# Kernel tuning notes

Measured on AMD Instinct MI355X. Metric: run time of the kernel, lower is better.

Reference implementation:

```python
import jax, jax.numpy as jnp
import numpy as np

N, DEG, IN_DIM, HID, OUT = 50000, 32, 256, 256, 128

def setup_inputs() -> dict:
    key = jax.random.key(0)
    k1, k2, k3, k4, k5, k6 = jax.random.split(key, 6)
    node_features = jax.random.normal(k1, (N, IN_DIM), dtype=jnp.float32)
    neighbor_idx = jax.random.randint(k2, (N, DEG), 0, N)
    scale1 = 1.0 / np.sqrt(2 * IN_DIM)
    scale2 = 1.0 / np.sqrt(HID)
    W1 = jax.random.normal(k3, (HID, 2 * IN_DIM), dtype=jnp.float32) * scale1
    b1 = jax.random.normal(k4, (HID,), dtype=jnp.float32) * scale1
    W2 = jax.random.normal(k5, (OUT, HID), dtype=jnp.float32) * scale2
    b2 = jax.random.normal(k6, (OUT,), dtype=jnp.float32) * scale2
    return {"node_features": node_features, "neighbor_idx": neighbor_idx,
            "W1": W1, "b1": b1, "W2": W2, "b2": b2}

def reference(node_features, neighbor_idx, W1, b1, W2, b2):
    # Layer 0 (mean aggregator, with neighbors):
    # gather [N, DEG, IN_DIM] neighbor features, mean over DEG
    nbr_mean = jnp.mean(node_features[neighbor_idx], axis=1)  # [N, IN_DIM]
    combined = jnp.concatenate([node_features, nbr_mean], axis=-1)  # [N, 2*IN_DIM]
    h = jax.nn.relu(combined @ W1.T + b1)  # [N, HID]
    # Layer 1: empty neighbor list -> linear_without_neighbors + relu
    out = jax.nn.relu(h @ W2.T + b2)  # [N, OUT]
    return out
```

## Files before the change

### kernel.cpp

```cpp
#include <hip/hip_runtime.h>
#include <stdint.h>

#define N_NODES 50000
#define DEG     32
#define IN_DIM  256
#define K1      512
#define HID     256
#define OUT_DIM 128

#define NCHUNK  4
#define CDIM    64
#define SLICE8  ((size_t)N_NODES * CDIM)
#define GT      16

#define MT2    64
#define NT2B   ((N_NODES + MT2 - 1) / MT2)
#define KC     64
#define HSTR2  264

typedef __bf16 bf16x8 __attribute__((ext_vector_type(8)));
typedef float  f32x4  __attribute__((ext_vector_type(4)));
typedef float  f32x2  __attribute__((ext_vector_type(2)));

__device__ __forceinline__ unsigned short f2bf(float f) {
    union { float f; unsigned u; } v; v.f = f;
    unsigned r = v.u + 0x7fffu + ((v.u >> 16) & 1u);
    return (unsigned short)(r >> 16);
}
__device__ __forceinline__ int clampN(int v) {
    return v < 0 ? 0 : (v >= N_NODES ? N_NODES - 1 : v);
}
__device__ __forceinline__ void async_copy16(const void* g, void* l) {
    __builtin_amdgcn_global_load_lds(
        (const __attribute__((address_space(1))) void*)g,
        (__attribute__((address_space(3))) void*)l, 16, 0, 0);
}

#define FEAT_BLKS ((N_NODES + 7) / 8)
__global__ __launch_bounds__(256)
void prep_all(const float* __restrict__ feat,
              const float* __restrict__ W1, const float* __restrict__ W2,
              const int*   __restrict__ nbr,
              unsigned short* __restrict__ featb,
              unsigned char*  __restrict__ featF8,
              unsigned short* __restrict__ W1b, unsigned short* __restrict__ W2b,
              unsigned short* __restrict__ nbr16)
{
    const int t = threadIdx.x;
    if (blockIdx.x < FEAT_BLKS) {
        const int node = blockIdx.x * 8 + (t >> 5);
        const int seg  = t & 31;
        if (node < N_NODES) {
            const float4* src = (const float4*)(feat + (size_t)node * IN_DIM + seg * 8);
            float4 f0 = src[0], f1 = src[1];
            ushort4 o0, o1;
            o0.x = f2bf(f0.x); o0.y = f2bf(f0.y); o0.z = f2bf(f0.z); o0.w = f2bf(f0.w);
            o1.x = f2bf(f1.x); o1.y = f2bf(f1.y); o1.z = f2bf(f1.z); o1.w = f2bf(f1.w);
            unsigned short* db = featb + (size_t)node * IN_DIM + seg * 8;
            *(ushort4*)db       = o0;
            *(ushort4*)(db + 4) = o1;
            int u0 = 0, u1 = 0;
            u0 = __builtin_amdgcn_cvt_pk_fp8_f32(f0.x, f0.y, u0, false);
            u0 = __builtin_amdgcn_cvt_pk_fp8_f32(f0.z, f0.w, u0, true);
            u1 = __builtin_amdgcn_cvt_pk_fp8_f32(f1.x, f1.y, u1, false);
            u1 = __builtin_amdgcn_cvt_pk_fp8_f32(f1.z, f1.w, u1, true);
            const int c   = seg >> 3;
            const int off = (seg & 7) * 8;
            unsigned char* d8 = featF8 + (size_t)c * SLICE8 + (size_t)node * CDIM + off;
            ((int*)d8)[0] = u0;
            ((int*)d8)[1] = u1;
        }
    } else {
        const int bid = blockIdx.x - FEAT_BLKS;
        const int stride = 256 * 256 * 4;
        const int tid4 = (bid * 256 + t) * 4;
        for (int i = tid4; i < HID * K1; i += stride) {
            float4 f = *(const float4*)(W1 + i);
            ushort4 o; o.x = f2bf(f.x); o.y = f2bf(f.y); o.z = f2bf(f.z); o.w = f2bf(f.w);
            *(ushort4*)(W1b + i) = o;
        }
        for (int i = tid4; i < OUT_DIM * HID; i += stride) {
            float4 f = *(const float4*)(W2 + i);
            ushort4 o; o.x = f2bf(f.x); o.y = f2bf(f.y); o.z = f2bf(f.z); o.w = f2bf(f.w);
            *(ushort4*)(W2b + i) = o;
        }
        for (int i = tid4; i < N_NODES * DEG; i += stride) {
            int4 v = *(const int4*)(nbr + i);
            ushort4 o;
            o.x = (unsigned short)clampN(v.x); o.y = (unsigned short)clampN(v.y);
            o.z = (unsigned short)clampN(v.z); o.w = (unsigned short)clampN(v.w);
            *(ushort4*)(nbr16 + i) = o;
        }
    }
}

__global__ __launch_bounds__(256)
void gather_mean_fp8(const unsigned char*  __restrict__ featF8,
                     const unsigned short* __restrict__ nbr16,
                     unsigned short*       __restrict__ meanb)
{
    __shared__ unsigned short sIdx[GT * DEG];
    const int tid  = threadIdx.x;
    const int c    = blockIdx.y;
    const int base = blockIdx.x * GT;

    if (tid < 128) {
        *(ushort4*)(sIdx + tid * 4) =
            *(const ushort4*)(nbr16 + (size_t)base * DEG + tid * 4);
    }
    __syncthreads();

    const unsigned char* slice = featF8 + (size_t)c * SLICE8;
    const int grp = tid >> 4;
    const int ln  = tid & 15;
    const unsigned short* idxr = sIdx + grp * DEG;

    unsigned vv[DEG];
    #pragma unroll
    for (int j = 0; j < DEG; ++j) {
        int nb = idxr[j];
        vv[j] = *(const unsigned*)(slice + (size_t)nb * CDIM + ln * 4);
    }
    float s0 = 0.f, s1 = 0.f, s2 = 0.f, s3 = 0.f;
    #pragma unroll
    for (int j = 0; j < DEG; ++j) {
        f32x2 lo = __builtin_amdgcn_cvt_pk_f32_fp8(vv[j], false);
        f32x2 hi = __builtin_amdgcn_cvt_pk_f32_fp8(vv[j], true);
        s0 += lo[0]; s1 += lo[1]; s2 += hi[0]; s3 += hi[1];
    }
    const float sc = 1.0f / 32.0f;
    ushort4 o;
    o.x = f2bf(s0 * sc); o.y = f2bf(s1 * sc);
    o.z = f2bf(s2 * sc); o.w = f2bf(s3 * sc);
    const int node = base + grp;
    *(ushort4*)(meanb + (size_t)node * IN_DIM + c * CDIM + ln * 4) = o;
}

__global__ __launch_bounds__(512, 2)
void sage_gemm2(const unsigned short* __restrict__ featb,
                const unsigned short* __restrict__ meanb,
                const unsigned short* __restrict__ W1b,
                const float*          __restrict__ b1,
                const unsigned short* __restrict__ W2b,
                const float*          __restrict__ b2,
                float*                __restrict__ out)
{
    __shared__ __align__(16) unsigned short sA[MT2 * KC];
    __shared__ __align__(16) unsigned short sW[256 * KC];
    __shared__ __align__(16) unsigned short sH[MT2 * HSTR2];

    const int tid  = threadIdx.x;
    const int lane = tid & 63;
    const int wave = tid >> 6;
    const int r    = lane & 15;
    const int q    = lane >> 4;
    const int mh   = wave >> 2;
    const int nq   = wave & 3;

    const int tbase = blockIdx.x * MT2;

    f32x4 acc1[2][4];
    #pragma unroll
    for (int mt = 0; mt < 2; ++mt)
        #pragma unroll
        for (int nt = 0; nt < 4; ++nt)
            acc1[mt][nt] = (f32x4){0.f, 0.f, 0.f, 0.f};

    for (int kc = 0; kc < 8; ++kc) {
        __syncthreads();
        {
            const int i = wave * 8 + (lane >> 3);
            const int node = clampN(tbase + i);
            const int g = (lane & 7) ^ (i & 7);
            const unsigned short* src = (kc < 4 ? featb : meanb)
                + (size_t)node * IN_DIM + (kc & 3) * KC + g * 8;
            async_copy16(src, &sA[wave * 8 * KC]);
        }
        #pragma unroll
        for (int j = 0; j < 4; ++j) {
            const int n = wave * 32 + j * 8 + (lane >> 3);
            const int g = (lane & 7) ^ (n & 7);
            async_copy16(W1b + (size_t)n * K1 + kc * KC + g * 8,
                         &sW[(wave * 32 + j * 8) * KC]);
        }
        __syncthreads();

        #pragma unroll
        for (int kk = 0; kk < 2; ++kk) {
            bf16x8 a[2], w[4];
            #pragma unroll
            for (int mt = 0; mt < 2; ++mt)
                a[mt] = *(const bf16x8*)(&sA[(mh * 32 + mt * 16 + r) * KC
                                             + ((kk * 4 + q) ^ (r & 7)) * 8]);
            #pragma unroll
            for (int nt = 0; nt < 4; ++nt)
                w[nt] = *(const bf16x8*)(&sW[(nq * 64 + nt * 16 + r) * KC
                                             + ((kk * 4 + q) ^ (r & 7)) * 8]);
            #pragma unroll
            for (int mt = 0; mt < 2; ++mt)
                #pragma unroll
                for (int nt = 0; nt < 4; ++nt)
                    acc1[mt][nt] = __builtin_amdgcn_mfma_f32_16x16x32_bf16(
                        a[mt], w[nt], acc1[mt][nt], 0, 0, 0);
        }
    }

    #pragma unroll
    for (int nt = 0; nt < 4; ++nt) {
        const int n = nq * 64 + nt * 16 + r;
        const float bias = b1[n];
        #pragma unroll
        for (int mt = 0; mt < 2; ++mt)
            #pragma unroll
            for (int g = 0; g < 4; ++g) {
                const int m = mh * 32 + mt * 16 + q * 4 + g;
                float v = acc1[mt][nt][g] + bias;
                sH[m * HSTR2 + n] = f2bf(v > 0.f ? v : 0.f);
            }
    }

    const int nh = wave & 3;
    f32x4 acc2[2][2];
    #pragma unroll
    for (int mt = 0; mt < 2; ++mt)
        #pragma unroll
        for (int nt = 0; nt < 2; ++nt)
            acc2[mt][nt] = (f32x4){0.f, 0.f, 0.f, 0.f};

    for (int kc = 0; kc < 4; ++kc) {
        __syncthreads();
        #pragma unroll
        for (int j = 0; j < 2; ++j) {
            const int n = wave * 16 + j * 8 + (lane >> 3);
            const int g = (lane & 7) ^ (n & 7);
            async_copy16(W2b + (size_t)n * HID + kc * KC + g * 8,
                         &sW[(wave * 16 + j * 8) * KC]);
        }
        __syncthreads();

        #pragma unroll
        for (int kk = 0; kk < 2; ++kk) {
            bf16x8 h[2], w[2];
            #pragma unroll
            for (int mt = 0; mt < 2; ++mt)
                h[mt] = *(const bf16x8*)(&sH[(mh * 32 + mt * 16 + r) * HSTR2
                                             + kc * KC + kk * 32 + q * 8]);
            #pragma unroll
            for (int nt = 0; nt < 2; ++nt)
                w[nt] = *(const bf16x8*)(&sW[(nh * 32 + nt * 16 + r) * KC
                                             + ((kk * 4 + q) ^ (r & 7)) * 8]);
            #pragma unroll
            for (int mt = 0; mt < 2; ++mt)
                #pragma unroll
                for (int nt = 0; nt < 2; ++nt)
                    acc2[mt][nt] = __builtin_amdgcn_mfma_f32_16x16x32_bf16(
                        h[mt], w[nt], acc2[mt][nt], 0, 0, 0);
        }
    }

    #pragma unroll
    for (int nt = 0; nt < 2; ++nt) {
        const int o = nh * 32 + nt * 16 + r;
        const float bias = b2[o];
        #pragma unroll
        for (int mt = 0; mt < 2; ++mt)
            #pragma unroll
            for (int g = 0; g < 4; ++g) {
                const int m = mh * 32 + mt * 16 + q * 4 + g;
                const int node = tbase + m;
                if (node < N_NODES) {
                    float v = acc2[mt][nt][g] + bias;
                    out[(size_t)node * OUT_DIM + o] = v > 0.f ? v : 0.f;
                }
            }
    }
}

__global__ __launch_bounds__(256)
void sage_naive(const float* __restrict__ feat, const int* __restrict__ nbr,
                const float* __restrict__ W1, const float* __restrict__ b1,
                const float* __restrict__ W2, const float* __restrict__ b2,
                float* __restrict__ out) {
    __shared__ float comb[K1];
    __shared__ float h[HID];
    const int node = blockIdx.x;
    const int t = threadIdx.x;
    comb[t] = feat[(size_t)node * IN_DIM + t];
    float acc = 0.f;
    for (int d = 0; d < DEG; ++d) {
        int nb = clampN(nbr[node * DEG + d]);
        acc += feat[(size_t)nb * IN_DIM + t];
    }
    comb[IN_DIM + t] = acc * (1.0f / 32.0f);
    __syncthreads();
    float s = b1[t];
    for (int k = 0; k < K1; ++k) s += comb[k] * W1[(size_t)t * K1 + k];
    h[t] = s > 0.f ? s : 0.f;
    __syncthreads();
    if (t < OUT_DIM) {
        float s2 = b2[t];
        for (int k = 0; k < HID; ++k) s2 += h[k] * W2[(size_t)t * HID + k];
        out[(size_t)node * OUT_DIM + t] = s2 > 0.f ? s2 : 0.f;
    }
}

extern "C" void kernel_launch(void* const* d_in, const int* in_sizes, int n_in,
                              void* d_out, int out_size, void* d_ws, size_t ws_size,
                              hipStream_t stream) {
    const float* feat = (const float*)d_in[0];
    const int*   nbr  = (const int*)d_in[1];
    const float* W1   = (const float*)d_in[2];
    const float* b1   = (const float*)d_in[3];
    const float* W2   = (const float*)d_in[4];
    const float* b2   = (const float*)d_in[5];
    float* out = (float*)d_out;

    const size_t feat_elems = (size_t)N_NODES * IN_DIM;
    const size_t w1_elems   = (size_t)HID * K1;
    const size_t w2_elems   = (size_t)OUT_DIM * HID;
    const size_t mean_elems = (size_t)N_NODES * IN_DIM;
    const size_t idx_elems  = (size_t)N_NODES * DEG;
    const size_t u16_elems  = feat_elems + w1_elems + w2_elems + mean_elems + idx_elems;
    const size_t need = u16_elems * sizeof(unsigned short)
                      + (size_t)NCHUNK * SLICE8;

    if (ws_size >= need) {
        unsigned short* featb  = (unsigned short*)d_ws;
        unsigned short* W1b    = featb + feat_elems;
        unsigned short* W2b    = W1b + w1_elems;
        unsigned short* meanb  = W2b + w2_elems;
        unsigned short* nbr16  = meanb + mean_elems;
        unsigned char*  featF8 = (unsigned char*)(nbr16 + idx_elems);

        prep_all<<<FEAT_BLKS + 256, 256, 0, stream>>>(feat, W1, W2, nbr,
                                                      featb, featF8, W1b, W2b, nbr16);
        gather_mean_fp8<<<dim3(N_NODES / GT, NCHUNK), 256, 0, stream>>>(featF8, nbr16, meanb);
        sage_gemm2<<<NT2B, 512, 0, stream>>>(featb, meanb, W1b, b1, W2b, b2, out);
    } else {
        sage_naive<<<N_NODES, 256, 0, stream>>>(feat, nbr, W1, b1, W2, b2, out);
    }
}
```

Measured before the change: 177.1 us.

## Double-buffer LDS staging in fused GEMM kernel with half-size K chunks

Restructures the fused two-layer GEMM to double-buffer its shared-memory tiles. K-chunks shrink from 64 to 32, so LDS use stays the same. The async global-to-LDS copies for the next chunk are issued before the MFMA work on the current chunk, leaving one barrier per iteration instead of two. The first W2 chunk is prefetched during the last layer-1 iteration. The aim is to hide global load latency behind compute, at the cost of twice as many loop iterations and barriers, with less compute per barrier.

```diff
diff --git a/kernel.cpp b/kernel.cpp
--- a/kernel.cpp
+++ b/kernel.cpp
@@ -15,7 +15,9 @@
 
 #define MT2    64
 #define NT2B   ((N_NODES + MT2 - 1) / MT2)
-#define KC     64
+#define KC2    32
+#define NKA    16
+#define NKB    8
 #define HSTR2  264
 
 typedef __bf16 bf16x8 __attribute__((ext_vector_type(8)));
@@ -137,7 +139,7 @@
 }
 
 __global__ __launch_bounds__(512, 2)
-void sage_gemm2(const unsigned short* __restrict__ featb,
+void sage_gemm3(const unsigned short* __restrict__ featb,
                 const unsigned short* __restrict__ meanb,
                 const unsigned short* __restrict__ W1b,
                 const float*          __restrict__ b1,
@@ -145,8 +147,8 @@
                 const float*          __restrict__ b2,
                 float*                __restrict__ out)
 {
-    __shared__ __align__(16) unsigned short sA[MT2 * KC];
-    __shared__ __align__(16) unsigned short sW[256 * KC];
+    __shared__ __align__(16) unsigned short sA[2][MT2 * KC2];
+    __shared__ __align__(16) unsigned short sW[2][256 * KC2];
     __shared__ __align__(16) unsigned short sH[MT2 * HSTR2];
 
     const int tid  = threadIdx.x;
@@ -156,8 +158,35 @@
     const int q    = lane >> 4;
     const int mh   = wave >> 2;
     const int nq   = wave & 3;
+    const int nh   = wave & 3;
 
     const int tbase = blockIdx.x * MT2;
+
+    const int srow = lane >> 2;
+    const int sg   = (lane & 3) ^ (srow & 3);
+
+    auto stageA = [&](int kc, int b) {
+        if (wave < 4) {
+            const int row  = wave * 16 + srow;
+            const int node = clampN(tbase + row);
+            const unsigned short* basep = (kc < 8) ? featb : meanb;
+            async_copy16(basep + (size_t)node * IN_DIM + (kc & 7) * KC2 + sg * 8,
+                         &sA[b][wave * 16 * KC2]);
+        }
+    };
+    auto stageW1 = [&](int kc, int b) {
+        #pragma unroll
+        for (int j = 0; j < 2; ++j) {
+            const int n = wave * 32 + j * 16 + srow;
+            async_copy16(W1b + (size_t)n * K1 + kc * KC2 + sg * 8,
+                         &sW[b][(wave * 32 + j * 16) * KC2]);
+        }
+    };
+    auto stageW2 = [&](int c, int b) {
+        const int n = wave * 16 + srow;
+        async_copy16(W2b + (size_t)n * HID + c * KC2 + sg * 8,
+                     &sW[b][(wave * 16) * KC2]);
+    };
 
     f32x4 acc1[2][4];
     #pragma unroll
@@ -166,36 +195,21 @@
         for (int nt = 0; nt < 4; ++nt)
             acc1[mt][nt] = (f32x4){0.f, 0.f, 0.f, 0.f};
 
-    for (int kc = 0; kc < 8; ++kc) {
-        __syncthreads();
+    stageA(0, 0); stageW1(0, 0);
+    __syncthreads();
+    int buf = 0;
+    for (int kc = 0; kc < NKA; ++kc) {
+        if (kc + 1 < NKA) { stageA(kc + 1, buf ^ 1); stageW1(kc + 1, buf ^ 1); }
+        else              { stageW2(0, buf ^ 1); }
         {
-            const int i = wave * 8 + (lane >> 3);
-            const int node = clampN(tbase + i);
-            const int g = (lane & 7) ^ (i & 7);
-            const unsigned short* src = (kc < 4 ? featb : meanb)
-                + (size_t)node * IN_DIM + (kc & 3) * KC + g * 8;
-            async_copy16(src, &sA[wave * 8 * KC]);
-        }
-        #pragma unroll
-        for (int j = 0; j < 4; ++j) {
-            const int n = wave * 32 + j * 8 + (lane >> 3);
-            const int g = (lane & 7) ^ (n & 7);
-            async_copy16(W1b + (size_t)n * K1 + kc * KC + g * 8,
-                         &sW[(wave * 32 + j * 8) * KC]);
-        }
-        __syncthreads();
-
-        #pragma unroll
-        for (int kk = 0; kk < 2; ++kk) {
+            const int sl = (q ^ (r & 3)) * 8;
             bf16x8 a[2], w[4];
             #pragma unroll
             for (int mt = 0; mt < 2; ++mt)
-                a[mt] = *(const bf16x8*)(&sA[(mh * 32 + mt * 16 + r) * KC
-                                             + ((kk * 4 + q) ^ (r & 7)) * 8]);
+                a[mt] = *(const bf16x8*)(&sA[buf][(mh * 32 + mt * 16 + r) * KC2 + sl]);
             #pragma unroll
             for (int nt = 0; nt < 4; ++nt)
-                w[nt] = *(const bf16x8*)(&sW[(nq * 64 + nt * 16 + r) * KC
-                                             + ((kk * 4 + q) ^ (r & 7)) * 8]);
+                w[nt] = *(const bf16x8*)(&sW[buf][(nq * 64 + nt * 16 + r) * KC2 + sl]);
             #pragma unroll
             for (int mt = 0; mt < 2; ++mt)
                 #pragma unroll
@@ -203,6 +217,8 @@
                     acc1[mt][nt] = __builtin_amdgcn_mfma_f32_16x16x32_bf16(
                         a[mt], w[nt], acc1[mt][nt], 0, 0, 0);
         }
+        __syncthreads();
+        buf ^= 1;
     }
 
     #pragma unroll
@@ -218,8 +234,8 @@
                 sH[m * HSTR2 + n] = f2bf(v > 0.f ? v : 0.f);
             }
     }
-
-    const int nh = wave & 3;
+    __syncthreads();
+
     f32x4 acc2[2][2];
     #pragma unroll
     for (int mt = 0; mt < 2; ++mt)
@@ -227,35 +243,27 @@
         for (int nt = 0; nt < 2; ++nt)
             acc2[mt][nt] = (f32x4){0.f, 0.f, 0.f, 0.f};
 
-    for (int kc = 0; kc < 4; ++kc) {
-        __syncthreads();
-        #pragma unroll
-        for (int j = 0; j < 2; ++j) {
-            const int n = wave * 16 + j * 8 + (lane >> 3);
-            const int g = (lane & 7) ^ (n & 7);
-            async_copy16(W2b + (size_t)n * HID + kc * KC + g * 8,
-                         &sW[(wave * 16 + j * 8) * KC]);
-        }
-        __syncthreads();
-
-        #pragma unroll
-        for (int kk = 0; kk < 2; ++kk) {
-            bf16x8 h[2], w[2];
+    for (int c = 0; c < NKB; ++c) {
+        if (c + 1 < NKB) stageW2(c + 1, buf ^ 1);
+        {
+            const int sl = (q ^ (r & 3)) * 8;
+            bf16x8 h[2], w2[2];
             #pragma unroll
             for (int mt = 0; mt < 2; ++mt)
                 h[mt] = *(const bf16x8*)(&sH[(mh * 32 + mt * 16 + r) * HSTR2
-                                             + kc * KC + kk * 32 + q * 8]);
+                                             + c * KC2 + q * 8]);
             #pragma unroll
             for (int nt = 0; nt < 2; ++nt)
-                w[nt] = *(const bf16x8*)(&sW[(nh * 32 + nt * 16 + r) * KC
-                                             + ((kk * 4 + q) ^ (r & 7)) * 8]);
+                w2[nt] = *(const bf16x8*)(&sW[buf][(nh * 32 + nt * 16 + r) * KC2 + sl]);
             #pragma unroll
             for (int mt = 0; mt < 2; ++mt)
                 #pragma unroll
                 for (int nt = 0; nt < 2; ++nt)
                     acc2[mt][nt] = __builtin_amdgcn_mfma_f32_16x16x32_bf16(
-                        h[mt], w[nt], acc2[mt][nt], 0, 0, 0);
-        }
+                        h[mt], w2[nt], acc2[mt][nt], 0, 0, 0);
+        }
+        __syncthreads();
+        buf ^= 1;
     }
 
     #pragma unroll
@@ -335,7 +343,7 @@
         prep_all<<<FEAT_BLKS + 256, 256, 0, stream>>>(feat, W1, W2, nbr,
                                                       featb, featF8, W1b, W2b, nbr16);
         gather_mean_fp8<<<dim3(N_NODES / GT, NCHUNK), 256, 0, stream>>>(featF8, nbr16, meanb);
-        sage_gemm2<<<NT2B, 512, 0, stream>>>(featb, meanb, W1b, b1, W2b, b2, out);
+        sage_gemm3<<<NT2B, 512, 0, stream>>>(featb, meanb, W1b, b1, W2b, b2, out);
     } else {
         sage_naive<<<N_NODES, 256, 0, stream>>>(feat, nbr, W1, b1, W2, b2, out);
     }
```

New measurement: 178.6 us. Within noise of the previous version (+0.9%).
